# Kernel tuning notes

Hardware: AMD Instinct MI355X
Metric: run time of the kernel (lower is better)

Reference implementation:

```python
import jax, jax.numpy as jnp
import numpy as np

DIM = 384
EPS = 1e-12  # F.normalize default eps


def setup_inputs() -> dict:
    key = jax.random.key(0)
    ks = jax.random.split(key, 6)
    b, c, h, w = 4, DIM, 64, 64
    x = jax.random.normal(ks[0], (b, c, h, w), dtype=jnp.float32)
    gamma = jnp.ones((c,), dtype=jnp.float32)  # WanRMS_norm gamma, init ones
    # 1x1 convs are per-pixel linear maps: [out_c, in_c] weight + bias
    w_qkv = jax.random.normal(ks[1], (3 * c, c), dtype=jnp.float32) * (1.0 / np.sqrt(c))
    b_qkv = jax.random.normal(ks[2], (3 * c,), dtype=jnp.float32) * 0.01
    w_proj = jax.random.normal(ks[3], (c, c), dtype=jnp.float32) * (1.0 / np.sqrt(c))
    b_proj = jax.random.normal(ks[4], (c,), dtype=jnp.float32) * 0.01
    return {"x": x, "gamma": gamma, "w_qkv": w_qkv, "b_qkv": b_qkv,
            "w_proj": w_proj, "b_proj": b_proj}


def reference(x, gamma, w_qkv, b_qkv, w_proj, b_proj):
    b, c, h, w = x.shape
    identity = x
    # WanRMS_norm: F.normalize over channel dim * sqrt(dim) * gamma
    l2 = jnp.sqrt(jnp.sum(x * x, axis=1, keepdims=True))
    xn = x / jnp.maximum(l2, EPS) * jnp.sqrt(jnp.float32(c)) * gamma[None, :, None, None]
    # 1x1 conv qkv: [b, 3c, h, w]
    qkv = jnp.einsum("bchw,oc->bohw", xn, w_qkv) + b_qkv[None, :, None, None]
    # flatten spatial -> tokens: [b, 3c, s] -> q/k/v each [b, s, c]
    s = h * w
    qkv = qkv.reshape(b, 3 * c, s).transpose(0, 2, 1)  # [b, s, 3c]
    q, k, v = jnp.split(qkv, 3, axis=-1)
    # single-head scaled dot-product attention (non-causal, as in Wan SDPA call)
    scores = jnp.einsum("bqc,bkc->bqk", q, k) / jnp.sqrt(jnp.float32(c))
    attn = jax.nn.softmax(scores, axis=-1)
    out = jnp.einsum("bqk,bkc->bqc", attn, v)  # [b, s, c]
    out = out.transpose(0, 2, 1).reshape(b, c, h, w)
    # 1x1 proj conv + residual
    out = jnp.einsum("bchw,oc->bohw", out, w_proj) + b_proj[None, :, None, None]
    return out + identity
```

## Files before the change

### kernel.cpp

```cpp
#include <hip/hip_runtime.h>
#include <cstdint>
#include <cstddef>

typedef __bf16 bf16;
typedef __bf16 bf16x8 __attribute__((ext_vector_type(8)));
typedef float  f32x4 __attribute__((ext_vector_type(4)));
typedef float  f32x16 __attribute__((ext_vector_type(16)));
typedef int    i32x4 __attribute__((ext_vector_type(4)));
typedef int    i32x8 __attribute__((ext_vector_type(8)));

#define MFMA16(a, b, c) __builtin_amdgcn_mfma_f32_16x16x32_bf16((a), (b), (c), 0, 0, 0)
#define MFMA_MX(a, b, c) \
    __builtin_amdgcn_mfma_scale_f32_32x32x64_f8f6f4((a), (b), (c), 0, 0, 0, 0x7F, 0, 0x7F)

#if __has_builtin(__builtin_amdgcn_exp2f)
#define EXP2(x) __builtin_amdgcn_exp2f(x)
#else
#define EXP2(x) exp2f(x)
#endif

__device__ __forceinline__ uint8_t to_fp8(float v) {
    return (uint8_t)(__builtin_amdgcn_cvt_pk_fp8_f32(v, v, 0, false) & 0xff);
}

__device__ __forceinline__ i32x8 ld32(const void* p) {
    i32x4 a = *(const i32x4*)p;
    i32x4 b = *(const i32x4*)((const char*)p + 16);
    i32x8 r;
    r[0] = a[0]; r[1] = a[1]; r[2] = a[2]; r[3] = a[3];
    r[4] = b[0]; r[5] = b[1]; r[6] = b[2]; r[7] = b[3];
    return r;
}

__device__ __forceinline__ void gload16(const void* g, void* l) {
    __builtin_amdgcn_global_load_lds(
        (const __attribute__((address_space(1))) unsigned int*)g,
        (__attribute__((address_space(3))) unsigned int*)l,
        16, 0, 0);
}

__global__ __launch_bounds__(256) void norm_kernel(
    const float* __restrict__ x, const float* __restrict__ gamma,
    const float* __restrict__ wqkv, const float* __restrict__ wproj,
    bf16* __restrict__ xn, bf16* __restrict__ wq, bf16* __restrict__ wp)
{
    const int tid = threadIdx.x;
    const int blk = blockIdx.x;
    if (blk >= 256) {
        int t0 = (blk - 256) * 256 + tid;
        for (int t = t0; t < 1152 * 384 + 384 * 384; t += 128 * 256) {
            if (t < 1152 * 384) wq[t] = (bf16)wqkv[t];
            else                wp[t - 1152 * 384] = (bf16)wproj[t - 1152 * 384];
        }
        return;
    }
    __shared__ float sG[384];
    __shared__ float sS[4][64];
    __shared__ float sScale[64];
    const int w = tid >> 6, l = tid & 63;
    for (int i = tid; i < 384; i += 256) sG[i] = gamma[i];
    const int b = blk >> 6, p0 = (blk & 63) << 6;
    const float* xb = x + ((size_t)b * 384) * 4096 + p0 + l;
    const float* xc = xb + (size_t)(96 * w) * 4096;
    float s0 = 0.f, s1 = 0.f;
#pragma unroll 8
    for (int c = 0; c < 96; c += 2) {
        float v0 = xc[(size_t)c * 4096];
        float v1 = xc[(size_t)(c + 1) * 4096];
        s0 += v0 * v0; s1 += v1 * v1;
    }
    sS[w][l] = s0 + s1;
    __syncthreads();
    if (w == 0) {
        float t = (sS[0][l] + sS[1][l]) + (sS[2][l] + sS[3][l]);
        sScale[l] = 19.595917942265423f / fmaxf(sqrtf(t), 1e-12f);
    }
    __syncthreads();
    float sc = sScale[l];
    int tok = (b << 12) + p0 + l;
    bf16* o = xn + (size_t)tok * 384 + 96 * w;
    for (int c0 = 0; c0 < 96; c0 += 8) {
        bf16x8 v8;
#pragma unroll
        for (int j = 0; j < 8; ++j)
            v8[j] = (bf16)(xc[(size_t)(c0 + j) * 4096] * sc * sG[96 * w + c0 + j]);
        *(bf16x8*)(o + c0) = v8;
    }
}

__device__ __forceinline__ void gemm_core_bt(
    bf16* sA, bf16* sB,
    const bf16* __restrict__ A, const bf16* __restrict__ B,
    const float* __restrict__ bias_m, const float* __restrict__ bias_n,
    uint8_t* __restrict__ Cout, const int mode, const int ldc,
    const int m0, const int n0)
{
    const int tid = threadIdx.x;
    const int l = tid & 63, w = tid >> 6;
    const int lo = l & 15, hi = l >> 4;
    const int wm = w >> 1, wn = w & 1;

    f32x4 acc[4][4] = {};

    for (int kt = 0; kt < 6; ++kt) {
        __syncthreads();
        const int k0 = kt * 64;
#pragma unroll
        for (int i = 0; i < 5; ++i) {
            int ci = i * 256 + tid;
            if (ci < 1152) {
                int row = ci / 9, off = ci % 9;
                gload16(A + (size_t)(m0 + row) * 384 + k0 + off * 8, (char*)sA + ci * 16);
                gload16(B + (size_t)(n0 + row) * 384 + k0 + off * 8, (char*)sB + ci * 16);
            }
        }
        __syncthreads();
#pragma unroll
        for (int ks = 0; ks < 2; ++ks) {
            bf16x8 af[4], bfr[4];
#pragma unroll
            for (int t = 0; t < 4; ++t)
                af[t] = *(const bf16x8*)(sA + (wm * 64 + t * 16 + lo) * 72 + ks * 32 + hi * 8);
#pragma unroll
            for (int t = 0; t < 4; ++t)
                bfr[t] = *(const bf16x8*)(sB + (wn * 64 + t * 16 + lo) * 72 + ks * 32 + hi * 8);
#pragma unroll
            for (int rt = 0; rt < 4; ++rt)
#pragma unroll
                for (int ct = 0; ct < 4; ++ct)
                    acc[rt][ct] = MFMA16(af[rt], bfr[ct], acc[rt][ct]);
        }
    }

#pragma unroll
    for (int rt = 0; rt < 4; ++rt) {
#pragma unroll
        for (int ct = 0; ct < 4; ++ct) {
            int mb = m0 + wm * 64 + rt * 16 + hi * 4;
            int n  = n0 + wn * 64 + ct * 16 + lo;
            if (mode == 0) {
                float bn = bias_n[n];
#pragma unroll
                for (int r = 0; r < 4; ++r)
                    Cout[(size_t)(mb + r) * ldc + n] = to_fp8(acc[rt][ct][r] + bn);
            } else {
#pragma unroll
                for (int r = 0; r < 4; ++r)
                    Cout[(size_t)(mb + r) * ldc + n] = to_fp8(acc[rt][ct][r] + bias_m[mb + r]);
            }
        }
    }
}

__global__ __launch_bounds__(256) void gemm_qkv(
    const bf16* __restrict__ xn, const bf16* __restrict__ wq,
    const float* __restrict__ b_qkv, uint8_t* __restrict__ qkb,
    uint8_t* __restrict__ vtb)
{
    __shared__ bf16 sA[128 * 72];
    __shared__ bf16 sB[128 * 72];
    const int id = blockIdx.x;
    if (id < 768) {
        const int xcd = id & 7, s = id >> 3;
        gemm_core_bt(sA, sB, xn, wq, nullptr, b_qkv, qkb, 0, 768,
                     (xcd * 16 + s / 6) * 128, (s % 6) * 128);
    } else {
        const int t = id - 768;
        const int xcd = t & 7, s = t >> 3;
        gemm_core_bt(sA, sB, wq + (size_t)768 * 384, xn, b_qkv + 768, nullptr,
                     vtb, 1, 16384, (s % 3) * 128, (xcd * 16 + s / 3) * 128);
    }
}

__global__ __launch_bounds__(256) void gemm_proj(
    const bf16* __restrict__ wp, const bf16* __restrict__ p0,
    const bf16* __restrict__ p1, const float* __restrict__ ml,
    const float* __restrict__ b_proj, const float* __restrict__ x,
    float* __restrict__ out)
{
    __shared__ bf16 sA[128 * 72];
    __shared__ bf16 sB[128 * 72];
    const int tid = threadIdx.x;
    const int l = tid & 63, w = tid >> 6;
    const int lo = l & 15, hi = l >> 4;
    const int wm = w >> 1, wn = w & 1;
    const int id = blockIdx.x;
    const int xcd = id & 7, s = id >> 3;
    const int m0 = (s % 3) * 128, n0 = (xcd * 16 + s / 3) * 128;

    f32x4 acc[4][4] = {};

    for (int kt = 0; kt < 6; ++kt) {
        __syncthreads();
        const int k0 = kt * 64;
#pragma unroll
        for (int i = 0; i < 5; ++i) {
            int ci = i * 256 + tid;
            if (ci < 1152) {
                int row = ci / 9, off = ci % 9;
                gload16(wp + (size_t)(m0 + row) * 384 + k0 + off * 8, (char*)sA + ci * 16);
                int tok = n0 + row;
                float2 ml0 = *(const float2*)(ml + (size_t)tok * 2);
                float2 ml1 = *(const float2*)(ml + (size_t)(16384 + tok) * 2);
                float mM = fmaxf(ml0.x, ml1.x);
                float a0 = EXP2(ml0.x - mM), a1 = EXP2(ml1.x - mM);
                float inv = 1.0f / (a0 * ml0.y + a1 * ml1.y);
                float w0 = a0 * inv, w1 = a1 * inv;
                size_t boff = (size_t)tok * 384 + k0 + off * 8;
                bf16x8 v0 = *(const bf16x8*)(p0 + boff);
                bf16x8 v1 = *(const bf16x8*)(p1 + boff);
                bf16x8 r;
#pragma unroll
                for (int j = 0; j < 8; ++j)
                    r[j] = (bf16)((float)v0[j] * w0 + (float)v1[j] * w1);
                *(bf16x8*)((char*)sB + ci * 16) = r;
            }
        }
        __syncthreads();
#pragma unroll
        for (int ks = 0; ks < 2; ++ks) {
            bf16x8 af[4], bfr[4];
#pragma unroll
            for (int t = 0; t < 4; ++t)
                af[t] = *(const bf16x8*)(sA + (wm * 64 + t * 16 + lo) * 72 + ks * 32 + hi * 8);
#pragma unroll
            for (int t = 0; t < 4; ++t)
                bfr[t] = *(const bf16x8*)(sB + (wn * 64 + t * 16 + lo) * 72 + ks * 32 + hi * 8);
#pragma unroll
            for (int rt = 0; rt < 4; ++rt)
#pragma unroll
                for (int ct = 0; ct < 4; ++ct)
                    acc[rt][ct] = MFMA16(af[rt], bfr[ct], acc[rt][ct]);
        }
    }

#pragma unroll
    for (int rt = 0; rt < 4; ++rt) {
#pragma unroll
        for (int ct = 0; ct < 4; ++ct) {
            int mb = m0 + wm * 64 + rt * 16 + hi * 4;
            int n  = n0 + wn * 64 + ct * 16 + lo;
            int bb = n >> 12, p = n & 4095;
#pragma unroll
            for (int r = 0; r < 4; ++r) {
                int m = mb + r;
                size_t idx = ((size_t)(bb * 384 + m)) * 4096 + p;
                out[idx] = acc[rt][ct][r] + b_proj[m] + x[idx];
            }
        }
    }
}

__global__ __launch_bounds__(256, 2) void flash_kernel(
    const uint8_t* __restrict__ qk, const uint8_t* __restrict__ vt,
    bf16* __restrict__ op0, bf16* __restrict__ op1, float* __restrict__ ml)
{
    extern __shared__ char smem[];
    uint8_t* sbase = (uint8_t*)smem;
    const int tid = threadIdx.x;
    const int l = tid & 63, w = tid >> 6;
    const int l31 = l & 31, hi2 = l >> 5;
    const int wq = w >> 1, wd = w & 1;
    const int id = blockIdx.x;
    const int qt = id >> 3, bh = id & 7;
    const int b = bh >> 1, half = bh & 1;
    const int q0 = b * 4096 + qt * 64;
    const int kvbase = b * 4096 + half * 2048;
    const float SC = 0.07362217057594547f;
    const float THR = 108.664f;

    uint32_t ksrc[7];
#pragma unroll
    for (int i = 0; i < 7; ++i) {
        int ci = i * 256 + tid;
        int row = ci / 25, off = ci % 25;
        ksrc[i] = (uint32_t)((kvbase + row) * 768 + 384 + off * 16);
    }
#pragma unroll
    for (int i = 0; i < 7; ++i) {
        if (i < 6 || tid < 64) gload16(qk + ksrc[i], sbase + i * 4096 + tid * 16);
        ksrc[i] += 49152;
    }

    uint32_t voff[6];
#pragma unroll
    for (int dt = 0; dt < 6; ++dt)
        voff[dt] = (uint32_t)((wd * 192 + dt * 32 + l31) * 16384 + kvbase + hi2 * 32);

    i32x8 qf[6];
    {
        const uint8_t* qrow = qk + (size_t)(q0 + wq * 32 + l31) * 768 + hi2 * 32;
#pragma unroll
        for (int ksw = 0; ksw < 6; ++ksw)
            qf[ksw] = ld32(qrow + ksw * 64);
    }

    f32x16 o[6] = {};
    float m = -1e30f, lsum = 0.f;

    __syncthreads();

    int c = 0;
    for (int kt = 0; kt < 32; ++kt) {
        if (kt < 31) {
            uint8_t* dst = sbase + (c ^ 1) * 25600;
#pragma unroll
            for (int i = 0; i < 7; ++i) {
                if (i < 6 || tid < 64) gload16(qk + ksrc[i], dst + i * 4096 + tid * 16);
                ksrc[i] += 49152;
            }
        }
        i32x8 av[6];
#pragma unroll
        for (int dt = 0; dt < 6; ++dt) {
            av[dt] = ld32(vt + voff[dt]);
            voff[dt] += 64;
        }

        const uint8_t* sK = sbase + c * 25600;
        f32x16 s0 = {}, s1 = {};
        __builtin_amdgcn_s_setprio(1);
#pragma unroll
        for (int ksw = 0; ksw < 6; ++ksw) {
            i32x8 ak0 = ld32(sK + (size_t)l31 * 400 + ksw * 64 + hi2 * 32);
            i32x8 ak1 = ld32(sK + (size_t)(32 + l31) * 400 + ksw * 64 + hi2 * 32);
            s0 = MFMA_MX(ak0, qf[ksw], s0);
            s1 = MFMA_MX(ak1, qf[ksw], s1);
        }
        __builtin_amdgcn_s_setprio(0);

        float a0 = fmaxf(fmaxf(s0[0],  s0[1]),  fmaxf(s0[2],  s0[3]));
        float a1 = fmaxf(fmaxf(s0[4],  s0[5]),  fmaxf(s0[6],  s0[7]));
        float a2 = fmaxf(fmaxf(s0[8],  s0[9]),  fmaxf(s0[10], s0[11]));
        float a3 = fmaxf(fmaxf(s0[12], s0[13]), fmaxf(s0[14], s0[15]));
        float b0 = fmaxf(fmaxf(s1[0],  s1[1]),  fmaxf(s1[2],  s1[3]));
        float b1 = fmaxf(fmaxf(s1[4],  s1[5]),  fmaxf(s1[6],  s1[7]));
        float b2 = fmaxf(fmaxf(s1[8],  s1[9]),  fmaxf(s1[10], s1[11]));
        float b3 = fmaxf(fmaxf(s1[12], s1[13]), fmaxf(s1[14], s1[15]));
        float mx = fmaxf(fmaxf(fmaxf(a0, a1), fmaxf(a2, a3)),
                         fmaxf(fmaxf(b0, b1), fmaxf(b2, b3)));
        mx = fmaxf(mx, __shfl_xor(mx, 32));
        if (__any(mx > m + THR)) {
            float mn = fmaxf(m, mx);
            float alpha = EXP2((m - mn) * SC);
            m = mn;
            lsum *= alpha;
#pragma unroll
            for (int dt = 0; dt < 6; ++dt)
#pragma unroll
                for (int r = 0; r < 16; ++r) o[dt][r] *= alpha;
        }
        float p0[16], p1[16];
        float msc = m * SC;
        float rsa = 0.f, rsb = 0.f, rsc = 0.f, rsd = 0.f;
#pragma unroll
        for (int r = 0; r < 16; r += 4) {
            p0[r]     = EXP2(fmaf(s0[r],     SC, -msc)); rsa += p0[r];
            p0[r + 1] = EXP2(fmaf(s0[r + 1], SC, -msc)); rsb += p0[r + 1];
            p0[r + 2] = EXP2(fmaf(s0[r + 2], SC, -msc)); rsc += p0[r + 2];
            p0[r + 3] = EXP2(fmaf(s0[r + 3], SC, -msc)); rsd += p0[r + 3];
        }
#pragma unroll
        for (int r = 0; r < 16; r += 4) {
            p1[r]     = EXP2(fmaf(s1[r],     SC, -msc)); rsa += p1[r];
            p1[r + 1] = EXP2(fmaf(s1[r + 1], SC, -msc)); rsb += p1[r + 1];
            p1[r + 2] = EXP2(fmaf(s1[r + 2], SC, -msc)); rsc += p1[r + 2];
            p1[r + 3] = EXP2(fmaf(s1[r + 3], SC, -msc)); rsd += p1[r + 3];
        }
        float rs = (rsa + rsb) + (rsc + rsd);
        rs += __shfl_xor(rs, 32);
        lsum += rs;

        int pk0[4], pk1[4];
#pragma unroll
        for (int i = 0; i < 4; ++i) {
            int d = __builtin_amdgcn_cvt_pk_fp8_f32(p0[4 * i], p0[4 * i + 1], 0, false);
            pk0[i] = __builtin_amdgcn_cvt_pk_fp8_f32(p0[4 * i + 2], p0[4 * i + 3], d, true);
            d = __builtin_amdgcn_cvt_pk_fp8_f32(p1[4 * i], p1[4 * i + 1], 0, false);
            pk1[i] = __builtin_amdgcn_cvt_pk_fp8_f32(p1[4 * i + 2], p1[4 * i + 3], d, true);
        }
        i32x8 pf;
#pragma unroll
        for (int i = 0; i < 4; ++i) {
            int x0 = __shfl_xor(pk0[i], 32);
            int x1 = __shfl_xor(pk1[i], 32);
            int own = hi2 ? pk1[i] : pk0[i];
            int oth = hi2 ? x1 : x0;
            pf[2 * i]     = hi2 ? oth : own;
            pf[2 * i + 1] = hi2 ? own : oth;
        }

        __builtin_amdgcn_s_setprio(1);
#pragma unroll
        for (int dt = 0; dt < 6; ++dt)
            o[dt] = MFMA_MX(av[dt], pf, o[dt]);
        __builtin_amdgcn_s_setprio(0);

        __syncthreads();
        c ^= 1;
    }

    float* tr = (float*)(smem + w * 4608);
    bf16* dst = half ? op1 : op0;
#pragma unroll
    for (int dt = 0; dt < 6; ++dt) {
#pragma unroll
        for (int r = 0; r < 16; ++r) {
            int d32 = (r & 3) + 8 * (r >> 2) + 4 * hi2;
            tr[l31 * 36 + d32] = o[dt][r];
        }
        f32x4 v0 = *(f32x4*)(tr + l31 * 36 + hi2 * 16 + 0);
        f32x4 v1 = *(f32x4*)(tr + l31 * 36 + hi2 * 16 + 4);
        f32x4 v2 = *(f32x4*)(tr + l31 * 36 + hi2 * 16 + 8);
        f32x4 v3 = *(f32x4*)(tr + l31 * 36 + hi2 * 16 + 12);
        bf16x8 h0, h1;
#pragma unroll
        for (int j = 0; j < 4; ++j) {
            h0[j] = (bf16)v0[j]; h0[4 + j] = (bf16)v1[j];
            h1[j] = (bf16)v2[j]; h1[4 + j] = (bf16)v3[j];
        }
        size_t tok = (size_t)(q0 + wq * 32 + l31);
        bf16* drow = dst + tok * 384 + wd * 192 + dt * 32 + hi2 * 16;
        *(bf16x8*)(drow + 0) = h0;
        *(bf16x8*)(drow + 8) = h1;
    }
    if (wd == 0 && hi2 == 0) {
        int tok = q0 + wq * 32 + l31;
        ml[(size_t)(half * 16384 + tok) * 2 + 0] = m * SC;
        ml[(size_t)(half * 16384 + tok) * 2 + 1] = lsum;
    }
}

extern "C" void kernel_launch(void* const* d_in, const int* in_sizes, int n_in,
                              void* d_out, int out_size, void* d_ws, size_t ws_size,
                              hipStream_t stream) {
    const float* x      = (const float*)d_in[0];
    const float* gamma  = (const float*)d_in[1];
    const float* w_qkv  = (const float*)d_in[2];
    const float* b_qkv  = (const float*)d_in[3];
    const float* w_proj = (const float*)d_in[4];
    const float* b_proj = (const float*)d_in[5];
    float* out = (float*)d_out;

    char* ws = (char*)d_ws;
    bf16* xn  = (bf16*)ws;    ws += (size_t)16384 * 384 * 2;
    uint8_t* qkb = (uint8_t*)ws; ws += (size_t)16384 * 768;
    uint8_t* vtb = (uint8_t*)ws; ws += (size_t)384 * 16384;
    bf16* ob  = (bf16*)ws;    ws += (size_t)16384 * 384 * 2;
    bf16* wqb = (bf16*)ws;    ws += (size_t)1152 * 384 * 2;
    bf16* wpb = (bf16*)ws;    ws += (size_t)384 * 384 * 2;
    float* mlb = (float*)ws;  ws += (size_t)2 * 16384 * 2 * 4;

    (void)hipFuncSetAttribute((const void*)flash_kernel,
                              hipFuncAttributeMaxDynamicSharedMemorySize, 51200);

    norm_kernel<<<384, 256, 0, stream>>>(x, gamma, w_qkv, w_proj, xn, wqb, wpb);
    gemm_qkv<<<1152, 256, 0, stream>>>(xn, wqb, b_qkv, qkb, vtb);
    flash_kernel<<<512, 256, 51200, stream>>>(qkb, vtb, xn, ob, mlb);
    gemm_proj<<<384, 256, 0, stream>>>(wpb, xn, ob, mlb, b_proj, x, out);
}
```

Before: 289.9 us.

## Split QK^T across wave pairs with LDS exchange of P and row stats

Result: faster. 274.7 us (-5.3%).

```diff
diff --git a/kernel.cpp b/kernel.cpp
--- a/kernel.cpp
+++ b/kernel.cpp
@@ -146,7 +146,8 @@
             } else {
 #pragma unroll
                 for (int r = 0; r < 4; ++r)
-                    Cout[(size_t)(mb + r) * ldc + n] = to_fp8(acc[rt][ct][r] + bias_m[mb + r]);
+                    Cout[(size_t)(n >> 6) * 24576 + (size_t)(mb + r) * 64 + (n & 63)]
+                        = to_fp8(acc[rt][ct][r] + bias_m[mb + r]);
             }
         }
     }
@@ -269,6 +270,10 @@
     const float SC = 0.07362217057594547f;
     const float THR = 108.664f;
 
+    uint32_t* Pl = (uint32_t*)(smem + 51200) + wq * 512;
+    float* mxb = (float*)(smem + 55296) + wq * 64;
+    float* smb = (float*)(smem + 55808) + wq * 64;
+
     uint32_t ksrc[7];
 #pragma unroll
     for (int i = 0; i < 7; ++i) {
@@ -285,7 +290,8 @@
     uint32_t voff[6];
 #pragma unroll
     for (int dt = 0; dt < 6; ++dt)
-        voff[dt] = (uint32_t)((wd * 192 + dt * 32 + l31) * 16384 + kvbase + hi2 * 32);
+        voff[dt] = (uint32_t)((kvbase >> 6) * 24576
+                              + (wd * 192 + dt * 32 + l31) * 64 + hi2 * 32);
 
     i32x8 qf[6];
     {
@@ -314,87 +320,83 @@
 #pragma unroll
         for (int dt = 0; dt < 6; ++dt) {
             av[dt] = ld32(vt + voff[dt]);
-            voff[dt] += 64;
+            voff[dt] += 24576;
         }
 
         const uint8_t* sK = sbase + c * 25600;
-        f32x16 s0 = {}, s1 = {};
+        f32x16 s = {};
         __builtin_amdgcn_s_setprio(1);
 #pragma unroll
         for (int ksw = 0; ksw < 6; ++ksw) {
-            i32x8 ak0 = ld32(sK + (size_t)l31 * 400 + ksw * 64 + hi2 * 32);
-            i32x8 ak1 = ld32(sK + (size_t)(32 + l31) * 400 + ksw * 64 + hi2 * 32);
-            s0 = MFMA_MX(ak0, qf[ksw], s0);
-            s1 = MFMA_MX(ak1, qf[ksw], s1);
+            i32x8 ak = ld32(sK + (size_t)(wd * 32 + l31) * 400 + ksw * 64 + hi2 * 32);
+            s = MFMA_MX(ak, qf[ksw], s);
         }
         __builtin_amdgcn_s_setprio(0);
 
-        float a0 = fmaxf(fmaxf(s0[0],  s0[1]),  fmaxf(s0[2],  s0[3]));
-        float a1 = fmaxf(fmaxf(s0[4],  s0[5]),  fmaxf(s0[6],  s0[7]));
-        float a2 = fmaxf(fmaxf(s0[8],  s0[9]),  fmaxf(s0[10], s0[11]));
-        float a3 = fmaxf(fmaxf(s0[12], s0[13]), fmaxf(s0[14], s0[15]));
-        float b0 = fmaxf(fmaxf(s1[0],  s1[1]),  fmaxf(s1[2],  s1[3]));
-        float b1 = fmaxf(fmaxf(s1[4],  s1[5]),  fmaxf(s1[6],  s1[7]));
-        float b2 = fmaxf(fmaxf(s1[8],  s1[9]),  fmaxf(s1[10], s1[11]));
-        float b3 = fmaxf(fmaxf(s1[12], s1[13]), fmaxf(s1[14], s1[15]));
-        float mx = fmaxf(fmaxf(fmaxf(a0, a1), fmaxf(a2, a3)),
-                         fmaxf(fmaxf(b0, b1), fmaxf(b2, b3)));
-        mx = fmaxf(mx, __shfl_xor(mx, 32));
-        if (__any(mx > m + THR)) {
-            float mn = fmaxf(m, mx);
-            float alpha = EXP2((m - mn) * SC);
-            m = mn;
-            lsum *= alpha;
-#pragma unroll
-            for (int dt = 0; dt < 6; ++dt)
-#pragma unroll
-                for (int r = 0; r < 16; ++r) o[dt][r] *= alpha;
-        }
-        float p0[16], p1[16];
+        float a0 = fmaxf(fmaxf(s[0],  s[1]),  fmaxf(s[2],  s[3]));
+        float a1 = fmaxf(fmaxf(s[4],  s[5]),  fmaxf(s[6],  s[7]));
+        float a2 = fmaxf(fmaxf(s[8],  s[9]),  fmaxf(s[10], s[11]));
+        float a3 = fmaxf(fmaxf(s[12], s[13]), fmaxf(s[14], s[15]));
+        float mxt = fmaxf(fmaxf(a0, a1), fmaxf(a2, a3));
+        mxt = fmaxf(mxt, __shfl_xor(mxt, 32));
+        mxb[wd * 32 + l31] = mxt;
+        if (kt == 0) {
+            __syncthreads();
+            m = fmaxf(mxt, mxb[(wd ^ 1) * 32 + l31]);
+        }
+
+        float p[16];
         float msc = m * SC;
         float rsa = 0.f, rsb = 0.f, rsc = 0.f, rsd = 0.f;
 #pragma unroll
         for (int r = 0; r < 16; r += 4) {
-            p0[r]     = EXP2(fmaf(s0[r],     SC, -msc)); rsa += p0[r];
-            p0[r + 1] = EXP2(fmaf(s0[r + 1], SC, -msc)); rsb += p0[r + 1];
-            p0[r + 2] = EXP2(fmaf(s0[r + 2], SC, -msc)); rsc += p0[r + 2];
-            p0[r + 3] = EXP2(fmaf(s0[r + 3], SC, -msc)); rsd += p0[r + 3];
-        }
-#pragma unroll
-        for (int r = 0; r < 16; r += 4) {
-            p1[r]     = EXP2(fmaf(s1[r],     SC, -msc)); rsa += p1[r];
-            p1[r + 1] = EXP2(fmaf(s1[r + 1], SC, -msc)); rsb += p1[r + 1];
-            p1[r + 2] = EXP2(fmaf(s1[r + 2], SC, -msc)); rsc += p1[r + 2];
-            p1[r + 3] = EXP2(fmaf(s1[r + 3], SC, -msc)); rsd += p1[r + 3];
-        }
-        float rs = (rsa + rsb) + (rsc + rsd);
-        rs += __shfl_xor(rs, 32);
-        lsum += rs;
-
-        int pk0[4], pk1[4];
+            p[r]     = EXP2(fmaf(s[r],     SC, -msc)); rsa += p[r];
+            p[r + 1] = EXP2(fmaf(s[r + 1], SC, -msc)); rsb += p[r + 1];
+            p[r + 2] = EXP2(fmaf(s[r + 2], SC, -msc)); rsc += p[r + 2];
+            p[r + 3] = EXP2(fmaf(s[r + 3], SC, -msc)); rsd += p[r + 3];
+        }
+        float tsum = (rsa + rsb) + (rsc + rsd);
+        tsum += __shfl_xor(tsum, 32);
+
+        int pk[4];
 #pragma unroll
         for (int i = 0; i < 4; ++i) {
-            int d = __builtin_amdgcn_cvt_pk_fp8_f32(p0[4 * i], p0[4 * i + 1], 0, false);
-            pk0[i] = __builtin_amdgcn_cvt_pk_fp8_f32(p0[4 * i + 2], p0[4 * i + 3], d, true);
-            d = __builtin_amdgcn_cvt_pk_fp8_f32(p1[4 * i], p1[4 * i + 1], 0, false);
-            pk1[i] = __builtin_amdgcn_cvt_pk_fp8_f32(p1[4 * i + 2], p1[4 * i + 3], d, true);
-        }
+            int d0 = __builtin_amdgcn_cvt_pk_fp8_f32(p[4 * i], p[4 * i + 1], 0, false);
+            pk[i] = __builtin_amdgcn_cvt_pk_fp8_f32(p[4 * i + 2], p[4 * i + 3], d0, true);
+        }
+#pragma unroll
+        for (int i = 0; i < 4; ++i)
+            Pl[(wd * 8 + 2 * i + hi2) * 32 + l31] = pk[i];
+        smb[wd * 32 + l31] = tsum;
+
+        __syncthreads();
+
+        float mx_o  = mxb[(wd ^ 1) * 32 + l31];
+        float sum_o = smb[(wd ^ 1) * 32 + l31];
         i32x8 pf;
 #pragma unroll
-        for (int i = 0; i < 4; ++i) {
-            int x0 = __shfl_xor(pk0[i], 32);
-            int x1 = __shfl_xor(pk1[i], 32);
-            int own = hi2 ? pk1[i] : pk0[i];
-            int oth = hi2 ? x1 : x0;
-            pf[2 * i]     = hi2 ? oth : own;
-            pf[2 * i + 1] = hi2 ? own : oth;
-        }
+        for (int j = 0; j < 8; ++j)
+            pf[j] = (int)Pl[(hi2 * 8 + j) * 32 + l31];
 
         __builtin_amdgcn_s_setprio(1);
 #pragma unroll
         for (int dt = 0; dt < 6; ++dt)
             o[dt] = MFMA_MX(av[dt], pf, o[dt]);
         __builtin_amdgcn_s_setprio(0);
+
+        float mc = fmaxf(mxt, mx_o);
+        if (__any(mc > m + THR)) {
+            float mn = fmaxf(m, mc);
+            float alpha = EXP2((m - mn) * SC);
+            m = mn;
+            lsum = (lsum + tsum + sum_o) * alpha;
+#pragma unroll
+            for (int dt = 0; dt < 6; ++dt)
+#pragma unroll
+                for (int r = 0; r < 16; ++r) o[dt][r] *= alpha;
+        } else {
+            lsum += tsum + sum_o;
+        }
 
         __syncthreads();
         c ^= 1;
@@ -452,10 +454,10 @@
     float* mlb = (float*)ws;  ws += (size_t)2 * 16384 * 2 * 4;
 
     (void)hipFuncSetAttribute((const void*)flash_kernel,
-                              hipFuncAttributeMaxDynamicSharedMemorySize, 51200);
+                              hipFuncAttributeMaxDynamicSharedMemorySize, 56320);
 
     norm_kernel<<<384, 256, 0, stream>>>(x, gamma, w_qkv, w_proj, xn, wqb, wpb);
     gemm_qkv<<<1152, 256, 0, stream>>>(xn, wqb, b_qkv, qkb, vtb);
-    flash_kernel<<<512, 256, 51200, stream>>>(qkb, vtb, xn, ob, mlb);
+    flash_kernel<<<512, 256, 56320, stream>>>(qkb, vtb, xn, ob, mlb);
     gemm_proj<<<384, 256, 0, stream>>>(wpb, xn, ob, mlb, b_proj, x, out);
 }
```

## Split flash attention KV into three slices and stage V through LDS

Applied to the files above, without the earlier changes.

Result: slower. 311.8 us (+7.5%).

```diff
diff --git a/kernel.cpp b/kernel.cpp
--- a/kernel.cpp
+++ b/kernel.cpp
@@ -144,9 +144,11 @@
                 for (int r = 0; r < 4; ++r)
                     Cout[(size_t)(mb + r) * ldc + n] = to_fp8(acc[rt][ct][r] + bn);
             } else {
+                size_t base = (size_t)(n >> 6) * 24576 + (size_t)((n >> 4) & 3) * 6144
+                            + (n & 15);
 #pragma unroll
                 for (int r = 0; r < 4; ++r)
-                    Cout[(size_t)(mb + r) * ldc + n] = to_fp8(acc[rt][ct][r] + bias_m[mb + r]);
+                    Cout[base + (size_t)(mb + r) * 16] = to_fp8(acc[rt][ct][r] + bias_m[mb + r]);
             }
         }
     }
@@ -174,9 +176,9 @@
 
 __global__ __launch_bounds__(256) void gemm_proj(
     const bf16* __restrict__ wp, const bf16* __restrict__ p0,
-    const bf16* __restrict__ p1, const float* __restrict__ ml,
-    const float* __restrict__ b_proj, const float* __restrict__ x,
-    float* __restrict__ out)
+    const bf16* __restrict__ p1, const bf16* __restrict__ p2,
+    const float* __restrict__ ml, const float* __restrict__ b_proj,
+    const float* __restrict__ x, float* __restrict__ out)
 {
     __shared__ bf16 sA[128 * 72];
     __shared__ bf16 sB[128 * 72];
@@ -202,17 +204,19 @@
                 int tok = n0 + row;
                 float2 ml0 = *(const float2*)(ml + (size_t)tok * 2);
                 float2 ml1 = *(const float2*)(ml + (size_t)(16384 + tok) * 2);
-                float mM = fmaxf(ml0.x, ml1.x);
-                float a0 = EXP2(ml0.x - mM), a1 = EXP2(ml1.x - mM);
-                float inv = 1.0f / (a0 * ml0.y + a1 * ml1.y);
-                float w0 = a0 * inv, w1 = a1 * inv;
+                float2 ml2 = *(const float2*)(ml + (size_t)(32768 + tok) * 2);
+                float mM = fmaxf(ml0.x, fmaxf(ml1.x, ml2.x));
+                float a0 = EXP2(ml0.x - mM), a1 = EXP2(ml1.x - mM), a2 = EXP2(ml2.x - mM);
+                float inv = 1.0f / (a0 * ml0.y + a1 * ml1.y + a2 * ml2.y);
+                float w0 = a0 * inv, w1 = a1 * inv, w2 = a2 * inv;
                 size_t boff = (size_t)tok * 384 + k0 + off * 8;
                 bf16x8 v0 = *(const bf16x8*)(p0 + boff);
                 bf16x8 v1 = *(const bf16x8*)(p1 + boff);
+                bf16x8 v2 = *(const bf16x8*)(p2 + boff);
                 bf16x8 r;
 #pragma unroll
                 for (int j = 0; j < 8; ++j)
-                    r[j] = (bf16)((float)v0[j] * w0 + (float)v1[j] * w1);
+                    r[j] = (bf16)((float)v0[j] * w0 + (float)v1[j] * w1 + (float)v2[j] * w2);
                 *(bf16x8*)((char*)sB + ci * 16) = r;
             }
         }
@@ -251,21 +255,26 @@
     }
 }
 
-__global__ __launch_bounds__(256, 2) void flash_kernel(
+__global__ __launch_bounds__(256, 3) void flash_kernel(
     const uint8_t* __restrict__ qk, const uint8_t* __restrict__ vt,
-    bf16* __restrict__ op0, bf16* __restrict__ op1, float* __restrict__ ml)
+    bf16* __restrict__ op0, bf16* __restrict__ op1, bf16* __restrict__ op2,
+    float* __restrict__ ml)
 {
     extern __shared__ char smem[];
-    uint8_t* sbase = (uint8_t*)smem;
+    uint8_t* sK = (uint8_t*)smem;
+    uint8_t* sV = (uint8_t*)smem + 25600;
     const int tid = threadIdx.x;
     const int l = tid & 63, w = tid >> 6;
     const int l31 = l & 31, hi2 = l >> 5;
     const int wq = w >> 1, wd = w & 1;
     const int id = blockIdx.x;
-    const int qt = id >> 3, bh = id & 7;
-    const int b = bh >> 1, half = bh & 1;
+    const int vidx = (id & 7) * 96 + (id >> 3);
+    const int g = vidx >> 6, qt = vidx & 63;
+    const int b = g / 3, sl = g - 3 * b;
+    const int nt = (sl == 0) ? 22 : 21;
+    const int tile0 = (sl == 0) ? 0 : 1 + 21 * sl;
     const int q0 = b * 4096 + qt * 64;
-    const int kvbase = b * 4096 + half * 2048;
+    const int kv0 = b * 4096 + tile0 * 64;
     const float SC = 0.07362217057594547f;
     const float THR = 108.664f;
 
@@ -274,18 +283,9 @@
     for (int i = 0; i < 7; ++i) {
         int ci = i * 256 + tid;
         int row = ci / 25, off = ci % 25;
-        ksrc[i] = (uint32_t)((kvbase + row) * 768 + 384 + off * 16);
-    }
-#pragma unroll
-    for (int i = 0; i < 7; ++i) {
-        if (i < 6 || tid < 64) gload16(qk + ksrc[i], sbase + i * 4096 + tid * 16);
-        ksrc[i] += 49152;
-    }
-
-    uint32_t voff[6];
-#pragma unroll
-    for (int dt = 0; dt < 6; ++dt)
-        voff[dt] = (uint32_t)((wd * 192 + dt * 32 + l31) * 16384 + kvbase + hi2 * 32);
+        ksrc[i] = (uint32_t)((kv0 + row) * 768 + 384 + off * 16);
+    }
+    uint32_t vbase = (uint32_t)((kv0 >> 6) * 24576 + tid * 16);
 
     i32x8 qf[6];
     {
@@ -298,26 +298,18 @@
     f32x16 o[6] = {};
     float m = -1e30f, lsum = 0.f;
 
-    __syncthreads();
-
-    int c = 0;
-    for (int kt = 0; kt < 32; ++kt) {
-        if (kt < 31) {
-            uint8_t* dst = sbase + (c ^ 1) * 25600;
-#pragma unroll
-            for (int i = 0; i < 7; ++i) {
-                if (i < 6 || tid < 64) gload16(qk + ksrc[i], dst + i * 4096 + tid * 16);
-                ksrc[i] += 49152;
-            }
-        }
-        i32x8 av[6];
-#pragma unroll
-        for (int dt = 0; dt < 6; ++dt) {
-            av[dt] = ld32(vt + voff[dt]);
-            voff[dt] += 64;
-        }
-
-        const uint8_t* sK = sbase + c * 25600;
+    for (int kt = 0; kt < nt; ++kt) {
+#pragma unroll
+        for (int i = 0; i < 7; ++i) {
+            if (i < 6 || tid < 64) gload16(qk + ksrc[i], sK + i * 4096 + tid * 16);
+            ksrc[i] += 49152;
+        }
+#pragma unroll
+        for (int i = 0; i < 6; ++i)
+            gload16(vt + vbase + i * 4096, sV + i * 4096 + tid * 16);
+        vbase += 24576;
+        __syncthreads();
+
         f32x16 s0 = {}, s1 = {};
         __builtin_amdgcn_s_setprio(1);
 #pragma unroll
@@ -392,16 +384,22 @@
 
         __builtin_amdgcn_s_setprio(1);
 #pragma unroll
-        for (int dt = 0; dt < 6; ++dt)
-            o[dt] = MFMA_MX(av[dt], pf, o[dt]);
+        for (int dt = 0; dt < 6; ++dt) {
+            int row = wd * 192 + dt * 32 + l31;
+            i32x4 alo = *(const i32x4*)(sV + hi2 * 12288 + row * 16);
+            i32x4 ahi = *(const i32x4*)(sV + hi2 * 12288 + 6144 + row * 16);
+            i32x8 av;
+            av[0] = alo[0]; av[1] = alo[1]; av[2] = alo[2]; av[3] = alo[3];
+            av[4] = ahi[0]; av[5] = ahi[1]; av[6] = ahi[2]; av[7] = ahi[3];
+            o[dt] = MFMA_MX(av, pf, o[dt]);
+        }
         __builtin_amdgcn_s_setprio(0);
 
         __syncthreads();
-        c ^= 1;
     }
 
     float* tr = (float*)(smem + w * 4608);
-    bf16* dst = half ? op1 : op0;
+    bf16* dst = (sl == 0) ? op0 : (sl == 1) ? op1 : op2;
 #pragma unroll
     for (int dt = 0; dt < 6; ++dt) {
 #pragma unroll
@@ -426,8 +424,8 @@
     }
     if (wd == 0 && hi2 == 0) {
         int tok = q0 + wq * 32 + l31;
-        ml[(size_t)(half * 16384 + tok) * 2 + 0] = m * SC;
-        ml[(size_t)(half * 16384 + tok) * 2 + 1] = lsum;
+        ml[(size_t)(sl * 16384 + tok) * 2 + 0] = m * SC;
+        ml[(size_t)(sl * 16384 + tok) * 2 + 1] = lsum;
     }
 }
 
@@ -447,15 +445,16 @@
     uint8_t* qkb = (uint8_t*)ws; ws += (size_t)16384 * 768;
     uint8_t* vtb = (uint8_t*)ws; ws += (size_t)384 * 16384;
     bf16* ob  = (bf16*)ws;    ws += (size_t)16384 * 384 * 2;
+    bf16* pc  = (bf16*)ws;    ws += (size_t)16384 * 384 * 2;
     bf16* wqb = (bf16*)ws;    ws += (size_t)1152 * 384 * 2;
     bf16* wpb = (bf16*)ws;    ws += (size_t)384 * 384 * 2;
-    float* mlb = (float*)ws;  ws += (size_t)2 * 16384 * 2 * 4;
+    float* mlb = (float*)ws;  ws += (size_t)3 * 16384 * 2 * 4;
 
     (void)hipFuncSetAttribute((const void*)flash_kernel,
-                              hipFuncAttributeMaxDynamicSharedMemorySize, 51200);
+                              hipFuncAttributeMaxDynamicSharedMemorySize, 50176);
 
     norm_kernel<<<384, 256, 0, stream>>>(x, gamma, w_qkv, w_proj, xn, wqb, wpb);
     gemm_qkv<<<1152, 256, 0, stream>>>(xn, wqb, b_qkv, qkb, vtb);
-    flash_kernel<<<512, 256, 51200, stream>>>(qkb, vtb, xn, ob, mlb);
-    gemm_proj<<<384, 256, 0, stream>>>(wpb, xn, ob, mlb, b_proj, x, out);
-}
+    flash_kernel<<<768, 256, 50176, stream>>>(qkb, vtb, xn, ob, pc, mlb);
+    gemm_proj<<<384, 256, 0, stream>>>(wpb, xn, ob, pc, mlb, b_proj, x, out);
+}
```

## Stage V tiles through LDS in flash kernel and vectorize norm loads

Applied to the files above, without the earlier changes.

Result: faster. 251.5 us (-13.3%).

```diff
diff --git a/kernel.cpp b/kernel.cpp
--- a/kernel.cpp
+++ b/kernel.cpp
@@ -46,8 +46,8 @@
 {
     const int tid = threadIdx.x;
     const int blk = blockIdx.x;
-    if (blk >= 256) {
-        int t0 = (blk - 256) * 256 + tid;
+    if (blk >= 64) {
+        int t0 = (blk - 64) * 256 + tid;
         for (int t = t0; t < 1152 * 384 + 384 * 384; t += 128 * 256) {
             if (t < 1152 * 384) wq[t] = (bf16)wqkv[t];
             else                wp[t - 1152 * 384] = (bf16)wproj[t - 1152 * 384];
@@ -55,36 +55,44 @@
         return;
     }
     __shared__ float sG[384];
-    __shared__ float sS[4][64];
-    __shared__ float sScale[64];
+    __shared__ f32x4 sS4[4][64];
+    __shared__ f32x4 sSc[64];
     const int w = tid >> 6, l = tid & 63;
     for (int i = tid; i < 384; i += 256) sG[i] = gamma[i];
-    const int b = blk >> 6, p0 = (blk & 63) << 6;
-    const float* xb = x + ((size_t)b * 384) * 4096 + p0 + l;
-    const float* xc = xb + (size_t)(96 * w) * 4096;
-    float s0 = 0.f, s1 = 0.f;
+    const int b = blk >> 4, p0 = (blk & 15) << 8;
+    const float* xw = x + ((size_t)(b * 384 + 96 * w)) * 4096 + p0 + 4 * l;
+    f32x4 ss = {};
 #pragma unroll 8
-    for (int c = 0; c < 96; c += 2) {
-        float v0 = xc[(size_t)c * 4096];
-        float v1 = xc[(size_t)(c + 1) * 4096];
-        s0 += v0 * v0; s1 += v1 * v1;
-    }
-    sS[w][l] = s0 + s1;
+    for (int c = 0; c < 96; ++c) {
+        f32x4 v = *(const f32x4*)(xw + (size_t)c * 4096);
+        ss += v * v;
+    }
+    sS4[w][l] = ss;
     __syncthreads();
     if (w == 0) {
-        float t = (sS[0][l] + sS[1][l]) + (sS[2][l] + sS[3][l]);
-        sScale[l] = 19.595917942265423f / fmaxf(sqrtf(t), 1e-12f);
+        f32x4 t = (sS4[0][l] + sS4[1][l]) + (sS4[2][l] + sS4[3][l]);
+        f32x4 sc;
+#pragma unroll
+        for (int j = 0; j < 4; ++j)
+            sc[j] = 19.595917942265423f / fmaxf(sqrtf(t[j]), 1e-12f);
+        sSc[l] = sc;
     }
     __syncthreads();
-    float sc = sScale[l];
-    int tok = (b << 12) + p0 + l;
-    bf16* o = xn + (size_t)tok * 384 + 96 * w;
+    f32x4 scv = sSc[l];
+    const int tokbase = (b << 12) + p0 + 4 * l;
     for (int c0 = 0; c0 < 96; c0 += 8) {
-        bf16x8 v8;
-#pragma unroll
-        for (int j = 0; j < 8; ++j)
-            v8[j] = (bf16)(xc[(size_t)(c0 + j) * 4096] * sc * sG[96 * w + c0 + j]);
-        *(bf16x8*)(o + c0) = v8;
+        f32x4 xv[8];
+#pragma unroll
+        for (int k = 0; k < 8; ++k)
+            xv[k] = *(const f32x4*)(xw + (size_t)(c0 + k) * 4096);
+#pragma unroll
+        for (int j = 0; j < 4; ++j) {
+            bf16x8 v8;
+#pragma unroll
+            for (int k = 0; k < 8; ++k)
+                v8[k] = (bf16)(xv[k][j] * scv[j] * sG[96 * w + c0 + k]);
+            *(bf16x8*)(xn + (size_t)(tokbase + j) * 384 + 96 * w + c0) = v8;
+        }
     }
 }
 
@@ -257,6 +265,7 @@
 {
     extern __shared__ char smem[];
     uint8_t* sbase = (uint8_t*)smem;
+    uint8_t* sV = sbase + 51200;
     const int tid = threadIdx.x;
     const int l = tid & 63, w = tid >> 6;
     const int l31 = l & 31, hi2 = l >> 5;
@@ -276,17 +285,19 @@
         int row = ci / 25, off = ci % 25;
         ksrc[i] = (uint32_t)((kvbase + row) * 768 + 384 + off * 16);
     }
+    uint32_t vsrc[8];
+#pragma unroll
+    for (int i = 0; i < 8; ++i) {
+        int ci = i * 256 + tid;
+        int row = ci / 5, off = ci % 5;
+        vsrc[i] = (uint32_t)(row * 16384 + kvbase + off * 16);
+    }
 #pragma unroll
     for (int i = 0; i < 7; ++i) {
         if (i < 6 || tid < 64) gload16(qk + ksrc[i], sbase + i * 4096 + tid * 16);
         ksrc[i] += 49152;
     }
 
-    uint32_t voff[6];
-#pragma unroll
-    for (int dt = 0; dt < 6; ++dt)
-        voff[dt] = (uint32_t)((wd * 192 + dt * 32 + l31) * 16384 + kvbase + hi2 * 32);
-
     i32x8 qf[6];
     {
         const uint8_t* qrow = qk + (size_t)(q0 + wq * 32 + l31) * 768 + hi2 * 32;
@@ -302,6 +313,11 @@
 
     int c = 0;
     for (int kt = 0; kt < 32; ++kt) {
+#pragma unroll
+        for (int i = 0; i < 8; ++i) {
+            if (i < 7 || tid < 128) gload16(vt + vsrc[i], sV + i * 4096 + tid * 16);
+            vsrc[i] += 64;
+        }
         if (kt < 31) {
             uint8_t* dst = sbase + (c ^ 1) * 25600;
 #pragma unroll
@@ -309,12 +325,6 @@
                 if (i < 6 || tid < 64) gload16(qk + ksrc[i], dst + i * 4096 + tid * 16);
                 ksrc[i] += 49152;
             }
-        }
-        i32x8 av[6];
-#pragma unroll
-        for (int dt = 0; dt < 6; ++dt) {
-            av[dt] = ld32(vt + voff[dt]);
-            voff[dt] += 64;
         }
 
         const uint8_t* sK = sbase + c * 25600;
@@ -390,10 +400,14 @@
             pf[2 * i + 1] = hi2 ? own : oth;
         }
 
+        __syncthreads();
+
         __builtin_amdgcn_s_setprio(1);
 #pragma unroll
-        for (int dt = 0; dt < 6; ++dt)
-            o[dt] = MFMA_MX(av[dt], pf, o[dt]);
+        for (int dt = 0; dt < 6; ++dt) {
+            i32x8 av = ld32(sV + (size_t)(wd * 192 + dt * 32 + l31) * 80 + hi2 * 32);
+            o[dt] = MFMA_MX(av, pf, o[dt]);
+        }
         __builtin_amdgcn_s_setprio(0);
 
         __syncthreads();
@@ -452,10 +466,10 @@
     float* mlb = (float*)ws;  ws += (size_t)2 * 16384 * 2 * 4;
 
     (void)hipFuncSetAttribute((const void*)flash_kernel,
-                              hipFuncAttributeMaxDynamicSharedMemorySize, 51200);
-
-    norm_kernel<<<384, 256, 0, stream>>>(x, gamma, w_qkv, w_proj, xn, wqb, wpb);
+                              hipFuncAttributeMaxDynamicSharedMemorySize, 81920);
+
+    norm_kernel<<<192, 256, 0, stream>>>(x, gamma, w_qkv, w_proj, xn, wqb, wpb);
     gemm_qkv<<<1152, 256, 0, stream>>>(xn, wqb, b_qkv, qkb, vtb);
-    flash_kernel<<<512, 256, 51200, stream>>>(qkb, vtb, xn, ob, mlb);
+    flash_kernel<<<512, 256, 81920, stream>>>(qkb, vtb, xn, ob, mlb);
     gemm_proj<<<384, 256, 0, stream>>>(wpb, xn, ob, mlb, b_proj, x, out);
 }
```
